# Performance work log

Measured on AMD Instinct MI355X. Metric: run time of the kernel, lower is better.

## Reference

```python
import jax, jax.numpy as jnp
import numpy as np

EMBED_DIM = 1024
NUM_HEADS = 16
HEAD_DIM = EMBED_DIM // NUM_HEADS
EPS = 1e-6
B, T = 4, 8192


def setup_inputs() -> dict:
    key = jax.random.key(0)
    ks = jax.random.split(key, 11)
    s = 1.0 / np.sqrt(EMBED_DIM)
    inp = {
        'query': jax.random.normal(ks[0], (B, T, EMBED_DIM), jnp.float32),
        'key': jax.random.normal(ks[1], (B, T, EMBED_DIM), jnp.float32),
        'value': jax.random.normal(ks[2], (B, T, EMBED_DIM), jnp.float32),
        'Wq': jax.random.normal(ks[3], (EMBED_DIM, EMBED_DIM), jnp.float32) * s,
        'bq': jnp.zeros((EMBED_DIM,), jnp.float32),
        'Wk': jax.random.normal(ks[4], (EMBED_DIM, EMBED_DIM), jnp.float32) * s,
        'bk': jnp.zeros((EMBED_DIM,), jnp.float32),
        'Wv': jax.random.normal(ks[5], (EMBED_DIM, EMBED_DIM), jnp.float32) * s,
        'bv': jnp.zeros((EMBED_DIM,), jnp.float32),
        'Wo': jax.random.normal(ks[6], (EMBED_DIM, EMBED_DIM), jnp.float32) * s,
        'bo': jnp.zeros((EMBED_DIM,), jnp.float32),
    }
    return inp


def _feature_map(x):
    return jax.nn.elu(x) + 1.0


def reference(query, key, value, Wq, bq, Wk, bk, Wv, bv, Wo, bo):
    b, t, _ = query.shape
    # projections (torch Linear: x @ W.T + b)
    q = query @ Wq.T + bq
    k = key @ Wk.T + bk
    v = value @ Wv.T + bv
    # split heads -> (b, h, t, d)
    def split(x):
        return x.reshape(b, t, NUM_HEADS, HEAD_DIM).transpose(0, 2, 1, 3)
    q = _feature_map(split(q))
    k = _feature_map(split(k))
    v = split(v)
    k_sum = k.sum(axis=2)                                   # (b,h,d)
    denom = jnp.einsum('bhtd,bhd->bht', q, k_sum) + EPS     # (b,h,t)
    kv = jnp.einsum('bhtd,bhtv->bhdv', k, v)                # (b,h,d,d)
    out = jnp.einsum('bhtd,bhde->bhte', q, kv) / denom[..., None]
    out = out.transpose(0, 2, 1, 3).reshape(b, t, EMBED_DIM)
    return out @ Wo.T + bo
```

## Files before the change

kernel.cpp:

```cpp
#include <hip/hip_runtime.h>
#include <hip/hip_bf16.h>

typedef long long TLONG;
typedef float  f32x4_t  __attribute__((ext_vector_type(4)));
typedef short  s16x8_t  __attribute__((ext_vector_type(8)));
typedef short  s16x4_t  __attribute__((ext_vector_type(4)));
typedef __bf16 bf16x8_t __attribute__((ext_vector_type(8)));

#define MDIM 32768
#define NDIM 1024
#define KDIM 1024
#define EPSV 1e-6f

__device__ __forceinline__ unsigned short f2bf_bits(float f) {
  __hip_bfloat16 h = __float2bfloat16(f);
  return __builtin_bit_cast(unsigned short, h);
}
__device__ __forceinline__ float bf2f(unsigned short u) {
  unsigned int x = ((unsigned int)u) << 16;
  return __builtin_bit_cast(float, x);
}
__device__ __forceinline__ void load_lds16(const void* g, void* l) {
  __builtin_amdgcn_global_load_lds((const __attribute__((address_space(1))) void*)g,
                                   (__attribute__((address_space(3))) void*)l, 16, 0, 0);
}

__global__ __launch_bounds__(256) void convert_f32_bf16(
    const float* __restrict__ in, unsigned short* __restrict__ out, TLONG n) {
  TLONG i = ((TLONG)blockIdx.x * blockDim.x + threadIdx.x) * 8;
  const TLONG stride = (TLONG)gridDim.x * blockDim.x * 8;
  for (; i < n; i += stride) {
    f32x4_t a = *reinterpret_cast<const f32x4_t*>(in + i);
    f32x4_t b = *reinterpret_cast<const f32x4_t*>(in + i + 4);
    s16x8_t o;
    o[0] = (short)f2bf_bits(a[0]); o[1] = (short)f2bf_bits(a[1]);
    o[2] = (short)f2bf_bits(a[2]); o[3] = (short)f2bf_bits(a[3]);
    o[4] = (short)f2bf_bits(b[0]); o[5] = (short)f2bf_bits(b[1]);
    o[6] = (short)f2bf_bits(b[2]); o[7] = (short)f2bf_bits(b[3]);
    *reinterpret_cast<s16x8_t*>(out + i) = o;
  }
}

template <int FMAP, int OUTF32>
__global__ __launch_bounds__(256) void gemm_bt(
    const unsigned short* __restrict__ A, const unsigned short* __restrict__ W,
    const float* __restrict__ bias, void* __restrict__ Cout) {
  const int bid = blockIdx.x;
  const int swz = (bid & 7) * 256 + (bid >> 3);
  const int mt = swz >> 3;
  const int nt = swz & 7;

  const int tid = threadIdx.x;
  const int lane = tid & 63;
  const int w = tid >> 6;
  const int wr = w >> 1, wc = w & 1;
  const int l15 = lane & 15, lh = lane >> 4;

  __shared__ short sA[128 * 32];
  __shared__ short sB[128 * 32];

  f32x4_t acc[4][4];
#pragma unroll
  for (int m = 0; m < 4; ++m)
#pragma unroll
    for (int n = 0; n < 4; ++n) acc[m][n] = (f32x4_t)0.0f;

  const int arow0 = mt * 128;
  const int brow0 = nt * 128;

  for (int kt = 0; kt < KDIM / 32; ++kt) {
    const int k0 = kt * 32;
#pragma unroll
    for (int i = 0; i < 2; ++i) {
      const int c = i * 256 + tid;
      const int r = c >> 2, s = c & 3;
      const int sg = s ^ ((r >> 1) & 3);
      load_lds16(A + ((arow0 + r) * KDIM + k0 + sg * 8), &sA[c * 8]);
    }
#pragma unroll
    for (int i = 0; i < 2; ++i) {
      const int c = i * 256 + tid;
      const int r = c >> 2, s = c & 3;
      const int sg = s ^ ((r >> 1) & 3);
      load_lds16(W + ((brow0 + r) * KDIM + k0 + sg * 8), &sB[c * 8]);
    }
    __syncthreads();
    bf16x8_t a[4], b[4];
#pragma unroll
    for (int m = 0; m < 4; ++m) {
      const int rA = wr * 64 + m * 16 + l15;
      const int sl = lh ^ ((rA >> 1) & 3);
      a[m] = __builtin_bit_cast(bf16x8_t,
          *reinterpret_cast<const s16x8_t*>(&sA[rA * 32 + sl * 8]));
    }
#pragma unroll
    for (int n = 0; n < 4; ++n) {
      const int rB = wc * 64 + n * 16 + l15;
      const int sl = lh ^ ((rB >> 1) & 3);
      b[n] = __builtin_bit_cast(bf16x8_t,
          *reinterpret_cast<const s16x8_t*>(&sB[rB * 32 + sl * 8]));
    }
#pragma unroll
    for (int m = 0; m < 4; ++m)
#pragma unroll
      for (int n = 0; n < 4; ++n)
        acc[m][n] = __builtin_amdgcn_mfma_f32_16x16x32_bf16(a[m], b[n], acc[m][n], 0, 0, 0);
    __syncthreads();
  }

#pragma unroll
  for (int n = 0; n < 4; ++n) {
    const int col = nt * 128 + wc * 64 + n * 16 + l15;
    const float bv = bias[col];
#pragma unroll
    for (int m = 0; m < 4; ++m) {
      const int row0 = mt * 128 + wr * 64 + m * 16 + lh * 4;
#pragma unroll
      for (int j = 0; j < 4; ++j) {
        float v = acc[m][n][j] + bv;
        if (FMAP) v = (v > 0.0f) ? (v + 1.0f) : __expf(v);
        if (OUTF32)
          reinterpret_cast<float*>(Cout)[(row0 + j) * NDIM + col] = v;
        else
          reinterpret_cast<unsigned short*>(Cout)[(row0 + j) * NDIM + col] = f2bf_bits(v);
      }
    }
  }
}

__global__ __launch_bounds__(256) void kv_ksum_kernel(
    const unsigned short* __restrict__ kf, const unsigned short* __restrict__ vf,
    float* __restrict__ kvT, float* __restrict__ ksum) {
  const int bid = blockIdx.x;
  const int bh = bid >> 3, ch = bid & 7;
  const int b = bh >> 4, h = bh & 15;
  const int tid = threadIdx.x;
  const int dg = tid >> 4, eg = tid & 15;
  __shared__ short sk[64 * 64];
  __shared__ short sv[64 * 64];
  float acc[4][4] = {};
  float ks[4] = {0.f, 0.f, 0.f, 0.f};
  const int rowbase = (b * 8192 + ch * 1024) * 1024 + h * 64;
  for (int tt = 0; tt < 1024; tt += 64) {
#pragma unroll
    for (int i = 0; i < 2; ++i) {
      const int c = i * 256 + tid;
      const int r = c >> 3, s = c & 7;
      load_lds16(kf + rowbase + (tt + r) * 1024 + s * 8, &sk[c * 8]);
      load_lds16(vf + rowbase + (tt + r) * 1024 + s * 8, &sv[c * 8]);
    }
    __syncthreads();
    for (int tl = 0; tl < 64; ++tl) {
      s16x4_t kr = *reinterpret_cast<const s16x4_t*>(&sk[tl * 64 + dg * 4]);
      s16x4_t vr = *reinterpret_cast<const s16x4_t*>(&sv[tl * 64 + eg * 4]);
      float kv4[4], vv4[4];
#pragma unroll
      for (int i = 0; i < 4; ++i) {
        kv4[i] = bf2f((unsigned short)kr[i]);
        vv4[i] = bf2f((unsigned short)vr[i]);
      }
#pragma unroll
      for (int i = 0; i < 4; ++i)
#pragma unroll
        for (int j = 0; j < 4; ++j) acc[i][j] += kv4[i] * vv4[j];
      if (eg == 0) {
#pragma unroll
        for (int i = 0; i < 4; ++i) ks[i] += kv4[i];
      }
    }
    __syncthreads();
  }
#pragma unroll
  for (int i = 0; i < 4; ++i) {
    if (eg == 0) atomicAdd(&ksum[bh * 64 + dg * 4 + i], ks[i]);
#pragma unroll
    for (int j = 0; j < 4; ++j)
      atomicAdd(&kvT[(bh * 64 + eg * 4 + j) * 64 + dg * 4 + i], acc[i][j]);
  }
}

__global__ __launch_bounds__(256) void attn_apply_kernel(
    const unsigned short* __restrict__ qf, const float* __restrict__ kvT,
    const float* __restrict__ ksum, unsigned short* __restrict__ att) {
  const int bid = blockIdx.x;
  const int swz = (bid & 7) * 256 + (bid >> 3);
  const int bh = swz >> 5;
  const int tile = swz & 31;
  const int b = bh >> 4, h = bh & 15;
  const int tid = threadIdx.x;
  const int lane = tid & 63, w = tid >> 6;
  const int l15 = lane & 15, lh = lane >> 4;

  float ksr[16];
#pragma unroll
  for (int i = 0; i < 16; ++i) ksr[i] = ksum[bh * 64 + lh * 16 + i];

  bf16x8_t bfrag[2][4];
#pragma unroll
  for (int ks2 = 0; ks2 < 2; ++ks2)
#pragma unroll
    for (int n = 0; n < 4; ++n) {
      const float* p = kvT + (bh * 64 + n * 16 + l15) * 64 + ks2 * 32 + lh * 8;
      f32x4_t p0 = *reinterpret_cast<const f32x4_t*>(p);
      f32x4_t p1 = *reinterpret_cast<const f32x4_t*>(p + 4);
      s16x8_t t;
      t[0] = (short)f2bf_bits(p0[0]); t[1] = (short)f2bf_bits(p0[1]);
      t[2] = (short)f2bf_bits(p0[2]); t[3] = (short)f2bf_bits(p0[3]);
      t[4] = (short)f2bf_bits(p1[0]); t[5] = (short)f2bf_bits(p1[1]);
      t[6] = (short)f2bf_bits(p1[2]); t[7] = (short)f2bf_bits(p1[3]);
      bfrag[ks2][n] = __builtin_bit_cast(bf16x8_t, t);
    }

  const int rbase = b * 8192 + tile * 256 + w * 64;
  f32x4_t acc[4][4];
#pragma unroll
  for (int m = 0; m < 4; ++m)
#pragma unroll
    for (int n = 0; n < 4; ++n) acc[m][n] = (f32x4_t)0.0f;
  float rden[4][4];

#pragma unroll
  for (int m = 0; m < 4; ++m) {
    const int row = rbase + m * 16 + l15;
    const unsigned short* qrow = qf + row * 1024 + h * 64;
    bf16x8_t afr[2];
#pragma unroll
    for (int ks2 = 0; ks2 < 2; ++ks2)
      afr[ks2] = __builtin_bit_cast(bf16x8_t,
          *reinterpret_cast<const s16x8_t*>(qrow + ks2 * 32 + lh * 8));
    s16x8_t qa = *reinterpret_cast<const s16x8_t*>(qrow + lh * 16);
    s16x8_t qb = *reinterpret_cast<const s16x8_t*>(qrow + lh * 16 + 8);
    float part = 0.f;
#pragma unroll
    for (int i = 0; i < 8; ++i) part += bf2f((unsigned short)qa[i]) * ksr[i];
#pragma unroll
    for (int i = 0; i < 8; ++i) part += bf2f((unsigned short)qb[i]) * ksr[8 + i];
    part += __shfl_xor(part, 16);
    part += __shfl_xor(part, 32);
#pragma unroll
    for (int j = 0; j < 4; ++j) {
      float dj = __shfl(part, lh * 4 + j);
      rden[m][j] = 1.0f / (dj + EPSV);
    }
#pragma unroll
    for (int ks2 = 0; ks2 < 2; ++ks2)
#pragma unroll
      for (int n = 0; n < 4; ++n)
        acc[m][n] = __builtin_amdgcn_mfma_f32_16x16x32_bf16(afr[ks2], bfrag[ks2][n], acc[m][n], 0, 0, 0);
  }

#pragma unroll
  for (int m = 0; m < 4; ++m)
#pragma unroll
    for (int n = 0; n < 4; ++n) {
      const int col = h * 64 + n * 16 + l15;
#pragma unroll
      for (int j = 0; j < 4; ++j) {
        const int row = rbase + m * 16 + lh * 4 + j;
        att[row * 1024 + col] = f2bf_bits(acc[m][n][j] * rden[m][j]);
      }
    }
}

extern "C" void kernel_launch(void* const* d_in, const int* in_sizes, int n_in,
                              void* d_out, int out_size, void* d_ws, size_t ws_size,
                              hipStream_t stream) {
  const float* query = (const float*)d_in[0];
  const float* key   = (const float*)d_in[1];
  const float* value = (const float*)d_in[2];
  const float* Wq = (const float*)d_in[3];
  const float* bq = (const float*)d_in[4];
  const float* Wk = (const float*)d_in[5];
  const float* bk = (const float*)d_in[6];
  const float* Wv = (const float*)d_in[7];
  const float* bv = (const float*)d_in[8];
  const float* Wo = (const float*)d_in[9];
  const float* bo = (const float*)d_in[10];
  float* out = (float*)d_out;

  if (ws_size < 277889024ULL) return;
  char* ws = (char*)d_ws;
  unsigned short* Vbf = (unsigned short*)(ws + 0);
  unsigned short* qf  = (unsigned short*)(ws + 67108864);
  unsigned short* kf  = (unsigned short*)(ws + 134217728);
  unsigned short* vf  = (unsigned short*)(ws + 201326592);
  unsigned short* Wqb = (unsigned short*)(ws + 268435456);
  unsigned short* Wkb = Wqb + 1048576;
  unsigned short* Wvb = Wkb + 1048576;
  unsigned short* Wob = Wvb + 1048576;
  float* kvT  = (float*)(ws + 276824064);

  unsigned short* Qbf = (unsigned short*)d_out;
  unsigned short* Kbf = Qbf + 33554432;

  hipMemsetAsync(kvT, 0, (size_t)(64 * 64 * 64 + 64 * 64) * sizeof(float), stream);

  convert_f32_bf16<<<2048, 256, 0, stream>>>(query, Qbf, 33554432LL);
  convert_f32_bf16<<<2048, 256, 0, stream>>>(key,   Kbf, 33554432LL);
  convert_f32_bf16<<<2048, 256, 0, stream>>>(value, Vbf, 33554432LL);
  convert_f32_bf16<<<512, 256, 0, stream>>>(Wq, Wqb, 1048576LL);
  convert_f32_bf16<<<512, 256, 0, stream>>>(Wk, Wkb, 1048576LL);
  convert_f32_bf16<<<512, 256, 0, stream>>>(Wv, Wvb, 1048576LL);
  convert_f32_bf16<<<512, 256, 0, stream>>>(Wo, Wob, 1048576LL);

  gemm_bt<1, 0><<<2048, 256, 0, stream>>>(Qbf, Wqb, bq, qf);
  gemm_bt<1, 0><<<2048, 256, 0, stream>>>(Kbf, Wkb, bk, kf);
  gemm_bt<0, 0><<<2048, 256, 0, stream>>>(Vbf, Wvb, bv, vf);

  kv_ksum_kernel<<<512, 256, 0, stream>>>(kf, vf, kvT, (float*)(ws + 277872640));

  attn_apply_kernel<<<2048, 256, 0, stream>>>(qf, kvT, (float*)(ws + 277872640), vf);

  gemm_bt<0, 1><<<2048, 256, 0, stream>>>(vf, Wob, bo, out);
}
```

Before: 691.5 us.

## Store K/V projections transposed and compute KV/ksum with MFMA

```diff
diff --git a/kernel.cpp b/kernel.cpp
--- a/kernel.cpp
+++ b/kernel.cpp
@@ -41,7 +41,7 @@
   }
 }
 
-template <int FMAP, int OUTF32>
+template <int FMAP, int OUT>
 __global__ __launch_bounds__(256) void gemm_bt(
     const unsigned short* __restrict__ A, const unsigned short* __restrict__ W,
     const float* __restrict__ bias, void* __restrict__ Cout) {
@@ -115,67 +115,96 @@
 #pragma unroll
     for (int m = 0; m < 4; ++m) {
       const int row0 = mt * 128 + wr * 64 + m * 16 + lh * 4;
-#pragma unroll
-      for (int j = 0; j < 4; ++j) {
-        float v = acc[m][n][j] + bv;
-        if (FMAP) v = (v > 0.0f) ? (v + 1.0f) : __expf(v);
-        if (OUTF32)
-          reinterpret_cast<float*>(Cout)[(row0 + j) * NDIM + col] = v;
-        else
-          reinterpret_cast<unsigned short*>(Cout)[(row0 + j) * NDIM + col] = f2bf_bits(v);
+      if (OUT == 2) {
+        const int b = row0 >> 13, tl = row0 & 8191;
+        const int h = col >> 6, d = col & 63;
+        s16x4_t o;
+#pragma unroll
+        for (int j = 0; j < 4; ++j) {
+          float v = acc[m][n][j] + bv;
+          if (FMAP) v = (v > 0.0f) ? (v + 1.0f) : __expf(v);
+          o[j] = (short)f2bf_bits(v);
+        }
+        *reinterpret_cast<s16x4_t*>(
+            reinterpret_cast<unsigned short*>(Cout) +
+            (((b * 16 + h) * 64 + d) * 8192 + tl)) = o;
+      } else {
+#pragma unroll
+        for (int j = 0; j < 4; ++j) {
+          float v = acc[m][n][j] + bv;
+          if (FMAP) v = (v > 0.0f) ? (v + 1.0f) : __expf(v);
+          if (OUT == 1)
+            reinterpret_cast<float*>(Cout)[(row0 + j) * NDIM + col] = v;
+          else
+            reinterpret_cast<unsigned short*>(Cout)[(row0 + j) * NDIM + col] = f2bf_bits(v);
+        }
       }
     }
   }
 }
 
-__global__ __launch_bounds__(256) void kv_ksum_kernel(
-    const unsigned short* __restrict__ kf, const unsigned short* __restrict__ vf,
+__global__ __launch_bounds__(256) void kv_ksum_mfma(
+    const unsigned short* __restrict__ kT, const unsigned short* __restrict__ vT,
     float* __restrict__ kvT, float* __restrict__ ksum) {
   const int bid = blockIdx.x;
-  const int bh = bid >> 3, ch = bid & 7;
-  const int b = bh >> 4, h = bh & 15;
+  const int bh = bid >> 4, ch = bid & 15;
   const int tid = threadIdx.x;
-  const int dg = tid >> 4, eg = tid & 15;
-  __shared__ short sk[64 * 64];
-  __shared__ short sv[64 * 64];
-  float acc[4][4] = {};
-  float ks[4] = {0.f, 0.f, 0.f, 0.f};
-  const int rowbase = (b * 8192 + ch * 1024) * 1024 + h * 64;
-  for (int tt = 0; tt < 1024; tt += 64) {
-#pragma unroll
-    for (int i = 0; i < 2; ++i) {
-      const int c = i * 256 + tid;
-      const int r = c >> 3, s = c & 7;
-      load_lds16(kf + rowbase + (tt + r) * 1024 + s * 8, &sk[c * 8]);
-      load_lds16(vf + rowbase + (tt + r) * 1024 + s * 8, &sv[c * 8]);
-    }
-    __syncthreads();
-    for (int tl = 0; tl < 64; ++tl) {
-      s16x4_t kr = *reinterpret_cast<const s16x4_t*>(&sk[tl * 64 + dg * 4]);
-      s16x4_t vr = *reinterpret_cast<const s16x4_t*>(&sv[tl * 64 + eg * 4]);
-      float kv4[4], vv4[4];
-#pragma unroll
-      for (int i = 0; i < 4; ++i) {
-        kv4[i] = bf2f((unsigned short)kr[i]);
-        vv4[i] = bf2f((unsigned short)vr[i]);
-      }
-#pragma unroll
-      for (int i = 0; i < 4; ++i)
-#pragma unroll
-        for (int j = 0; j < 4; ++j) acc[i][j] += kv4[i] * vv4[j];
-      if (eg == 0) {
-#pragma unroll
-        for (int i = 0; i < 4; ++i) ks[i] += kv4[i];
-      }
-    }
-    __syncthreads();
-  }
-#pragma unroll
-  for (int i = 0; i < 4; ++i) {
-    if (eg == 0) atomicAdd(&ksum[bh * 64 + dg * 4 + i], ks[i]);
-#pragma unroll
-    for (int j = 0; j < 4; ++j)
-      atomicAdd(&kvT[(bh * 64 + eg * 4 + j) * 64 + dg * 4 + i], acc[i][j]);
+  const int lane = tid & 63, w = tid >> 6;
+  const int l15 = lane & 15, lh = lane >> 4;
+  const int dblk = (w >> 1) * 32, eblk = (w & 1) * 32;
+
+  f32x4_t acc[2][2];
+#pragma unroll
+  for (int m = 0; m < 2; ++m)
+#pragma unroll
+    for (int n = 0; n < 2; ++n) acc[m][n] = (f32x4_t)0.0f;
+  float ks0 = 0.f, ks1 = 0.f;
+
+  const int tbase = ch * 512 + lh * 8;
+  const unsigned short* ka = kT + (bh * 64 + dblk + l15) * 8192 + tbase;
+  const unsigned short* va = vT + (bh * 64 + eblk + l15) * 8192 + tbase;
+
+  for (int t0 = 0; t0 < 512; t0 += 32) {
+    s16x8_t ar[2], br[2];
+#pragma unroll
+    for (int m = 0; m < 2; ++m)
+      ar[m] = *reinterpret_cast<const s16x8_t*>(ka + m * 16 * 8192 + t0);
+#pragma unroll
+    for (int n = 0; n < 2; ++n)
+      br[n] = *reinterpret_cast<const s16x8_t*>(va + n * 16 * 8192 + t0);
+#pragma unroll
+    for (int m = 0; m < 2; ++m)
+#pragma unroll
+      for (int n = 0; n < 2; ++n)
+        acc[m][n] = __builtin_amdgcn_mfma_f32_16x16x32_bf16(
+            __builtin_bit_cast(bf16x8_t, ar[m]),
+            __builtin_bit_cast(bf16x8_t, br[n]), acc[m][n], 0, 0, 0);
+    if (eblk == 0) {
+#pragma unroll
+      for (int i = 0; i < 8; ++i) ks0 += bf2f((unsigned short)ar[0][i]);
+#pragma unroll
+      for (int i = 0; i < 8; ++i) ks1 += bf2f((unsigned short)ar[1][i]);
+    }
+  }
+
+  if (eblk == 0) {
+    ks0 += __shfl_xor(ks0, 16); ks0 += __shfl_xor(ks0, 32);
+    ks1 += __shfl_xor(ks1, 16); ks1 += __shfl_xor(ks1, 32);
+    if (lh == 0) {
+      atomicAdd(&ksum[bh * 64 + dblk + l15], ks0);
+      atomicAdd(&ksum[bh * 64 + dblk + 16 + l15], ks1);
+    }
+  }
+#pragma unroll
+  for (int n = 0; n < 2; ++n) {
+    const int e = eblk + n * 16 + l15;
+#pragma unroll
+    for (int m = 0; m < 2; ++m) {
+      const int d0 = dblk + m * 16 + lh * 4;
+#pragma unroll
+      for (int j = 0; j < 4; ++j)
+        atomicAdd(&kvT[(bh * 64 + e) * 64 + d0 + j], acc[m][n][j]);
+    }
   }
 }
 
@@ -282,13 +311,14 @@
   char* ws = (char*)d_ws;
   unsigned short* Vbf = (unsigned short*)(ws + 0);
   unsigned short* qf  = (unsigned short*)(ws + 67108864);
-  unsigned short* kf  = (unsigned short*)(ws + 134217728);
-  unsigned short* vf  = (unsigned short*)(ws + 201326592);
+  unsigned short* kTf = (unsigned short*)(ws + 134217728);
+  unsigned short* vTf = (unsigned short*)(ws + 201326592);
   unsigned short* Wqb = (unsigned short*)(ws + 268435456);
   unsigned short* Wkb = Wqb + 1048576;
   unsigned short* Wvb = Wkb + 1048576;
   unsigned short* Wob = Wvb + 1048576;
   float* kvT  = (float*)(ws + 276824064);
+  float* ksum = (float*)(ws + 277872640);
 
   unsigned short* Qbf = (unsigned short*)d_out;
   unsigned short* Kbf = Qbf + 33554432;
@@ -304,12 +334,12 @@
   convert_f32_bf16<<<512, 256, 0, stream>>>(Wo, Wob, 1048576LL);
 
   gemm_bt<1, 0><<<2048, 256, 0, stream>>>(Qbf, Wqb, bq, qf);
-  gemm_bt<1, 0><<<2048, 256, 0, stream>>>(Kbf, Wkb, bk, kf);
-  gemm_bt<0, 0><<<2048, 256, 0, stream>>>(Vbf, Wvb, bv, vf);
-
-  kv_ksum_kernel<<<512, 256, 0, stream>>>(kf, vf, kvT, (float*)(ws + 277872640));
-
-  attn_apply_kernel<<<2048, 256, 0, stream>>>(qf, kvT, (float*)(ws + 277872640), vf);
-
-  gemm_bt<0, 1><<<2048, 256, 0, stream>>>(vf, Wob, bo, out);
-}
+  gemm_bt<1, 2><<<2048, 256, 0, stream>>>(Kbf, Wkb, bk, kTf);
+  gemm_bt<0, 2><<<2048, 256, 0, stream>>>(Vbf, Wvb, bv, vTf);
+
+  kv_ksum_mfma<<<1024, 256, 0, stream>>>(kTf, vTf, kvT, ksum);
+
+  attn_apply_kernel<<<2048, 256, 0, stream>>>(qf, kvT, ksum, Vbf);
+
+  gemm_bt<0, 1><<<2048, 256, 0, stream>>>(Vbf, Wob, bo, out);
+}
```

New measurement: 674.3 us. 2.5% less time.
